# Kernel optimization log

Measured on AMD Instinct MI355X. Metric: run time of the kernel, lower is better.

Reference implementation:

```python
import jax, jax.numpy as jnp
import numpy as np

B = 256      # graph pairs
N = 256      # nodes per graph (uniform -> padding is a reshape)
DEG = 16     # avg degree
D = 32       # one_hot_dim
F1, F2, F3 = 128, 64, 64
T = 16       # tensor_neurons
BINS = 16
BOT = 16     # bottle_neck_neurons


def setup_inputs() -> dict:
    key = jax.random.key(0)
    ks = jax.random.split(key, 24)
    NT = B * N            # total nodes per side
    NE = B * N * DEG      # total directed edges per side
    x_q = jax.random.normal(ks[0], (NT, D), jnp.float32)
    x_c = jax.random.normal(ks[1], (NT, D), jnp.float32)
    edge_q = jax.random.randint(ks[2], (2, NE), 0, NT, jnp.int32)
    edge_c = jax.random.randint(ks[3], (2, NE), 0, NT, jnp.int32)
    qgraph_sizes = jnp.full((B,), N, jnp.int32)
    cgraph_sizes = jnp.full((B,), N, jnp.int32)

    def glorot(k, shape):
        fan = sum(shape[-2:]) if len(shape) >= 2 else shape[0] * 2
        return jax.random.uniform(k, shape, jnp.float32, -1.0, 1.0) * np.sqrt(6.0 / fan)

    params = dict(
        W1=glorot(ks[4], (D, F1)), b1=jnp.zeros((F1,), jnp.float32),
        W2=glorot(ks[5], (F1, F2)), b2=jnp.zeros((F2,), jnp.float32),
        W3=glorot(ks[6], (F2, F3)), b3=jnp.zeros((F3,), jnp.float32),
        attn_w=glorot(ks[7], (F3, F3)),
        ntn_a_w=glorot(ks[8], (T, F3, F3)),
        ntn_b_w=glorot(ks[9], (2 * F3, T)),
        ntn_bias=glorot(ks[10], (T, 1)),
        fc1_w=glorot(ks[11], (T + BINS, BOT)), fc1_b=jnp.zeros((BOT,), jnp.float32),
        fc2_w=glorot(ks[12], (BOT, 1)), fc2_b=jnp.zeros((1,), jnp.float32),
    )
    return dict(x_q=x_q, edge_q=edge_q, x_c=x_c, edge_c=edge_c,
                qgraph_sizes=qgraph_sizes, cgraph_sizes=cgraph_sizes, **params)


def _gcn(x, src, dst, W, b):
    n = x.shape[0]
    h = x @ W
    loop = jnp.arange(n, dtype=src.dtype)
    s = jnp.concatenate([src, loop])
    d = jnp.concatenate([dst, loop])
    deg = jax.ops.segment_sum(jnp.ones(s.shape, h.dtype), d, num_segments=n)
    dinv = jnp.where(deg > 0, jax.lax.rsqrt(jnp.maximum(deg, 1.0)), 0.0)
    coef = (dinv[s] * dinv[d])[:, None]
    return jax.ops.segment_sum(h[s] * coef, d, num_segments=n) + b


def _gnn(x, ei, W1, b1, W2, b2, W3, b3):
    src, dst = ei[0], ei[1]
    h = jax.nn.relu(_gcn(x, src, dst, W1, b1))        # dropout is identity in eval
    h = jax.nn.relu(_gcn(h, src, dst, W2, b2))
    return _gcn(h, src, dst, W3, b3)                  # [B*N, F3]


def _att_pool(q, attn_w, sizes):
    # q: [B, N, F3]
    ctx = jnp.tanh((q.sum(axis=1) @ attn_w) / sizes.astype(q.dtype)[:, None])  # [B, F3]
    sig = jax.nn.sigmoid(jnp.einsum('bnf,bf->bn', q, ctx))                      # [B, N]
    return jnp.einsum('bnf,bn->bf', q, sig)                                     # [B, F3]


def _pair_hist(q, c):
    # per-pair histogram of q @ c^T with BINS bins over each pair's [min, max]
    s = jax.lax.stop_gradient(jnp.einsum('bnf,bmf->bnm', q, c))  # [B, N, N]
    mn = s.min(axis=(1, 2), keepdims=True)
    mx = s.max(axis=(1, 2), keepdims=True)
    idx = jnp.clip(jnp.floor((s - mn) / jnp.maximum(mx - mn, 1e-12) * BINS),
                   0, BINS - 1).astype(jnp.int32)
    gid = (idx + jnp.arange(B, dtype=jnp.int32)[:, None, None] * BINS).reshape(-1)
    h = jax.ops.segment_sum(jnp.ones(gid.shape, jnp.float32), gid,
                            num_segments=B * BINS).reshape(B, BINS)
    return h / h.sum(axis=1, keepdims=True)


def reference(x_q, edge_q, x_c, edge_c, qgraph_sizes, cgraph_sizes,
              W1, b1, W2, b2, W3, b3, attn_w, ntn_a_w, ntn_b_w, ntn_bias,
              fc1_w, fc1_b, fc2_w, fc2_b):
    q = _gnn(x_q, edge_q, W1, b1, W2, b2, W3, b3).reshape(B, N, F3)
    c = _gnn(x_c, edge_c, W1, b1, W2, b2, W3, b3).reshape(B, N, F3)
    e1 = _att_pool(q, attn_w, qgraph_sizes)
    e2 = _att_pool(c, attn_w, cgraph_sizes)
    ntn = (jnp.einsum('bi,tij,bj->bt', e1, ntn_a_w, e2)
           + jnp.concatenate([e1, e2], axis=-1) @ ntn_b_w
           + ntn_bias[:, 0])
    scores = jax.nn.relu(ntn)                                   # [B, T]
    hist = _pair_hist(q, c)                                     # [B, BINS]
    scores = jnp.concatenate([scores, hist], axis=1)
    scores = jax.nn.relu(scores @ fc1_w + fc1_b)
    p = jax.nn.sigmoid(scores @ fc2_w + fc2_b)[:, 0]            # [B]
    ged = -0.5 * (qgraph_sizes + cgraph_sizes).astype(p.dtype) * jnp.log(p)
    return ged
```

## Files before the change

### kernel.cpp

```cpp
#include <hip/hip_runtime.h>
#include <hip/hip_bf16.h>
#include <math.h>

#define BB 256
#define NN 256
#define NT (BB*NN)
#define NT2 (2*NT)
#define NE (NT*16)
#define DD 32
#define F1C 128
#define F2C 64
#define F3C 64
#define TT 16
#define BINS 16

#define NBUCK 256
#define BSHIFT 9
#define BNODES 512
#define BCAP 10240
#define EPB 4096

typedef __attribute__((ext_vector_type(8))) short short8;
typedef __attribute__((ext_vector_type(4))) float f32x4;
typedef __attribute__((ext_vector_type(2))) float f32x2;

__device__ inline float b2f(ushort u) { return __uint_as_float(((uint)u) << 16); }
__device__ inline ushort f2b(float f) {
    uint u = __float_as_uint(f);
    return (ushort)((u + 0x7fffu + ((u >> 16) & 1u)) >> 16);
}
__device__ inline float clamp8(float v) { return fminf(fmaxf(v, -448.0f), 448.0f); }
__device__ inline uchar f2f8(float v) {
    int r = __builtin_amdgcn_cvt_pk_fp8_f32(clamp8(v), 0.0f, 0, false);
    return (uchar)(r & 0xff);
}
__device__ inline void f8x8_acc(uint2 w, float* acc) {
    f32x2 p;
    p = __builtin_amdgcn_cvt_pk_f32_fp8(w.x, false); acc[0] += p.x; acc[1] += p.y;
    p = __builtin_amdgcn_cvt_pk_f32_fp8(w.x, true);  acc[2] += p.x; acc[3] += p.y;
    p = __builtin_amdgcn_cvt_pk_f32_fp8(w.y, false); acc[4] += p.x; acc[5] += p.y;
    p = __builtin_amdgcn_cvt_pk_f32_fp8(w.y, true);  acc[6] += p.x; acc[7] += p.y;
}
__device__ inline uint2 f8x8_pack(const float* v) {
    uint2 r;
    r.x = (uint)__builtin_amdgcn_cvt_pk_fp8_f32(clamp8(v[0]), clamp8(v[1]), 0, false);
    r.x = (uint)__builtin_amdgcn_cvt_pk_fp8_f32(clamp8(v[2]), clamp8(v[3]), (int)r.x, true);
    r.y = (uint)__builtin_amdgcn_cvt_pk_fp8_f32(clamp8(v[4]), clamp8(v[5]), 0, false);
    r.y = (uint)__builtin_amdgcn_cvt_pk_fp8_f32(clamp8(v[6]), clamp8(v[7]), (int)r.y, true);
    return r;
}

__global__ __launch_bounds__(256) void zero_k(int* __restrict__ gcount) {
    gcount[threadIdx.x] = 0;
}

__global__ __launch_bounds__(256) void csr_p1_k(const int* __restrict__ eq, const int* __restrict__ ec,
                                                uint* __restrict__ staged, int* __restrict__ gcount) {
    __shared__ uint s_pk[EPB];
    __shared__ int s_cnt[NBUCK];
    __shared__ int s_off[NBUCK];
    __shared__ int s_base[NBUCK];
    __shared__ int s_gb[NBUCK];
    int t = threadIdx.x;
    bool sideB = blockIdx.x >= 256;
    const int* edge = sideB ? ec : eq;
    int off = sideB ? NT : 0;
    int e0 = (blockIdx.x & 255) * EPB;
    s_cnt[t] = 0;
    __syncthreads();
    uint pk[16]; int bk[16];
#pragma unroll
    for (int j = 0; j < 16; j++) {
        int e = e0 + j * 256 + t;
        int s = edge[e] + off;
        int d = edge[NE + e] + off;
        bk[j] = d >> BSHIFT;
        pk[j] = ((uint)s << BSHIFT) | (uint)(d & (BNODES - 1));
        atomicAdd(&s_cnt[bk[j]], 1);
    }
    __syncthreads();
    s_off[t] = s_cnt[t];
    __syncthreads();
    for (int o = 1; o < NBUCK; o <<= 1) {
        int x = (t >= o) ? s_off[t - o] : 0;
        __syncthreads();
        s_off[t] += x;
        __syncthreads();
    }
    {
        int ex = s_off[t] - s_cnt[t];
        s_base[t] = ex;
        s_off[t] = ex;
        s_gb[t] = atomicAdd(&gcount[t], s_cnt[t]);
    }
    __syncthreads();
#pragma unroll
    for (int j = 0; j < 16; j++) {
        int pos = atomicAdd(&s_off[bk[j]], 1);
        s_pk[pos] = pk[j];
    }
    __syncthreads();
    int w = t >> 6, l = t & 63;
    int bsel = l >> 4, l16 = l & 15;
    for (int pb = w; pb < NBUCK / 4; pb += 4) {
        int b = pb * 4 + bsel;
        int n = s_cnt[b], st = s_base[b], gb = s_gb[b];
        if (gb + n > BCAP) n = max(0, BCAP - gb);
        for (int i = l16; i < n; i += 16)
            staged[b * BCAP + gb + i] = s_pk[st + i];
    }
}

__global__ __launch_bounds__(256) void csr_p2_k(const uint* __restrict__ staged, const int* __restrict__ gcount,
                                                int* __restrict__ rp, int* __restrict__ indeg,
                                                float* __restrict__ dinv, int* __restrict__ ep) {
    int b = blockIdx.x;
    int t = threadIdx.x;
    __shared__ int cnt[BNODES];
    __shared__ int fl[BNODES];
    __shared__ int wsum[256];
    __shared__ int gsc[NBUCK];
    cnt[t] = 0; cnt[t + 256] = 0;
    gsc[t] = min(gcount[t], BCAP);
    __syncthreads();
    for (int off = 1; off < NBUCK; off <<= 1) {
        int x = (t >= off) ? gsc[t - off] : 0;
        __syncthreads();
        gsc[t] += x;
        __syncthreads();
    }
    int gbase = (b == 0) ? 0 : gsc[b - 1];
    int n = min(gcount[b], BCAP);
    const uint* sb = staged + (size_t)b * BCAP;
    int i = t;
    for (; i + 768 < n; i += 1024) {
        uint p0 = sb[i];
        uint p1 = sb[i + 256];
        uint p2 = sb[i + 512];
        uint p3 = sb[i + 768];
        atomicAdd(&cnt[p0 & (BNODES - 1)], 1);
        atomicAdd(&cnt[p1 & (BNODES - 1)], 1);
        atomicAdd(&cnt[p2 & (BNODES - 1)], 1);
        atomicAdd(&cnt[p3 & (BNODES - 1)], 1);
    }
    for (; i < n; i += 256)
        atomicAdd(&cnt[sb[i] & (BNODES - 1)], 1);
    __syncthreads();
    int base2 = t * 2;
    int c0 = cnt[base2], c1 = cnt[base2 + 1];
    int s2 = c0 + c1;
    wsum[t] = s2;
    __syncthreads();
    for (int off = 1; off < 256; off <<= 1) {
        int x = (t >= off) ? wsum[t - off] : 0;
        __syncthreads();
        wsum[t] += x;
        __syncthreads();
    }
    int p = gbase + wsum[t] - s2;
    int v0 = b * BNODES + base2;
    rp[v0] = p;          fl[base2] = p;
    indeg[v0] = c0;      dinv[v0] = rsqrtf((float)(c0 + 1));
    p += c0;
    rp[v0 + 1] = p;      fl[base2 + 1] = p;
    indeg[v0 + 1] = c1;  dinv[v0 + 1] = rsqrtf((float)(c1 + 1));
    __syncthreads();
    i = t;
    for (; i + 768 < n; i += 1024) {
        uint p0 = sb[i];
        uint p1 = sb[i + 256];
        uint p2 = sb[i + 512];
        uint p3 = sb[i + 768];
        ep[atomicAdd(&fl[p0 & (BNODES - 1)], 1)] = (int)(p0 >> BSHIFT);
        ep[atomicAdd(&fl[p1 & (BNODES - 1)], 1)] = (int)(p1 >> BSHIFT);
        ep[atomicAdd(&fl[p2 & (BNODES - 1)], 1)] = (int)(p2 >> BSHIFT);
        ep[atomicAdd(&fl[p3 & (BNODES - 1)], 1)] = (int)(p3 >> BSHIFT);
    }
    for (; i < n; i += 256) {
        uint pk = sb[i];
        ep[atomicAdd(&fl[pk & (BNODES - 1)], 1)] = (int)(pk >> BSHIFT);
    }
}

__global__ __launch_bounds__(256) void cvt2w_k(const float* __restrict__ a, const float* __restrict__ b,
                                               const float* __restrict__ dinv, ushort* __restrict__ out,
                                               const float* __restrict__ W1, const float* __restrict__ W2,
                                               const float* __restrict__ W3, ushort* __restrict__ Wt1,
                                               ushort* __restrict__ Wt2, uchar* __restrict__ Wt3f8) {
    const int NB_X = NT2 * DD / 4 / 256;
    if (blockIdx.x < NB_X) {
        int i = blockIdx.x * 256 + threadIdx.x;
        const int per = NT * DD / 4;
        bool sideB = i >= per;
        const float4* src = (const float4*)(sideB ? b : a);
        float4 v = src[sideB ? i - per : i];
        float dv = dinv[i / (DD / 4)];
        ushort4 o;
        o.x = f2b(v.x * dv); o.y = f2b(v.y * dv); o.z = f2b(v.z * dv); o.w = f2b(v.w * dv);
        ((ushort4*)out)[i] = o;
    } else {
        int i = (blockIdx.x - NB_X) * 256 + threadIdx.x;
        if (i < DD * F1C)  { int k = i / F1C, n = i % F1C; Wt1[n * DD + k]  = f2b(W1[i]); }
        if (i < F1C * F2C) { int k = i / F2C, n = i % F2C; Wt2[n * F1C + k] = f2b(W2[i]); }
        if (i < F2C * F3C) { int k = i / F3C, n = i % F3C; Wt3f8[n * F2C + k] = f2f8(W3[i]); }
    }
}

template<int F, bool BIAS, bool RELU>
__global__ __launch_bounds__(256) void agg_bf_k(const ushort* __restrict__ in, const int* __restrict__ rp,
                                                const int* __restrict__ indeg, const int* __restrict__ ep,
                                                const float* __restrict__ dinv,
                                                const float* __restrict__ bias, ushort* __restrict__ out) {
    constexpr int LPV = F / 8;
    constexpr int VPB = 256 / LPV;
    int g = threadIdx.x / LPV;
    int l = threadIdx.x % LPV;
    int v = blockIdx.x * VPB + g;
    float dv = dinv[v];
    short8 rs = *(const short8*)(in + (size_t)v * F + l * 8);
    float acc[8];
#pragma unroll
    for (int j = 0; j < 8; j++) acc[j] = b2f((ushort)rs[j]);
    int start = rp[v];
    int cnt   = indeg[v];
    int i = 0;
    for (; i + 4 <= cnt; i += 4) {
        int s0 = ep[start + i];
        int s1 = ep[start + i + 1];
        int s2 = ep[start + i + 2];
        int s3 = ep[start + i + 3];
        short8 r0 = *(const short8*)(in + (size_t)s0 * F + l * 8);
        short8 r1 = *(const short8*)(in + (size_t)s1 * F + l * 8);
        short8 r2 = *(const short8*)(in + (size_t)s2 * F + l * 8);
        short8 r3 = *(const short8*)(in + (size_t)s3 * F + l * 8);
#pragma unroll
        for (int j = 0; j < 8; j++) {
            acc[j] += b2f((ushort)r0[j]);
            acc[j] += b2f((ushort)r1[j]);
            acc[j] += b2f((ushort)r2[j]);
            acc[j] += b2f((ushort)r3[j]);
        }
    }
    for (; i < cnt; i++) {
        int s0 = ep[start + i];
        short8 r0 = *(const short8*)(in + (size_t)s0 * F + l * 8);
#pragma unroll
        for (int j = 0; j < 8; j++) acc[j] += b2f((ushort)r0[j]);
    }
    short8 o;
#pragma unroll
    for (int j = 0; j < 8; j++) {
        float x = dv * acc[j];
        if (BIAS) x += bias[l * 8 + j];
        if (RELU) x = fmaxf(x, 0.0f);
        o[j] = (short)f2b(x);
    }
    *(short8*)(out + (size_t)v * F + l * 8) = o;
}

template<bool OUT_BF16, bool BIAS, bool RELU>
__global__ __launch_bounds__(256) void agg_f8_k(const uchar* __restrict__ in, const int* __restrict__ rp,
                                                const int* __restrict__ indeg, const int* __restrict__ ep,
                                                const float* __restrict__ dinv,
                                                const float* __restrict__ bias, void* __restrict__ outp) {
    int g = threadIdx.x >> 3;
    int l = threadIdx.x & 7;
    int v = blockIdx.x * 32 + g;
    float dv = dinv[v];
    float acc[8] = {0, 0, 0, 0, 0, 0, 0, 0};
    f8x8_acc(*(const uint2*)(in + (size_t)v * 64 + l * 8), acc);
    int start = rp[v];
    int cnt   = indeg[v];
    int i = 0;
    for (; i + 4 <= cnt; i += 4) {
        int s0 = ep[start + i];
        int s1 = ep[start + i + 1];
        int s2 = ep[start + i + 2];
        int s3 = ep[start + i + 3];
        uint2 g0 = *(const uint2*)(in + (size_t)s0 * 64 + l * 8);
        uint2 g1 = *(const uint2*)(in + (size_t)s1 * 64 + l * 8);
        uint2 g2 = *(const uint2*)(in + (size_t)s2 * 64 + l * 8);
        uint2 g3 = *(const uint2*)(in + (size_t)s3 * 64 + l * 8);
        f8x8_acc(g0, acc); f8x8_acc(g1, acc); f8x8_acc(g2, acc); f8x8_acc(g3, acc);
    }
    for (; i < cnt; i++) {
        int s0 = ep[start + i];
        f8x8_acc(*(const uint2*)(in + (size_t)s0 * 64 + l * 8), acc);
    }
#pragma unroll
    for (int j = 0; j < 8; j++) {
        float x = dv * acc[j];
        if (BIAS) x += bias[l * 8 + j];
        if (RELU) x = fmaxf(x, 0.0f);
        acc[j] = x;
    }
    if (OUT_BF16) {
        short8 o;
#pragma unroll
        for (int j = 0; j < 8; j++) o[j] = (short)f2b(acc[j]);
        *(short8*)((ushort*)outp + (size_t)v * 64 + l * 8) = o;
    } else {
        *(uint2*)((uchar*)outp + (size_t)v * 64 + l * 8) = f8x8_pack(acc);
    }
}

__global__ __launch_bounds__(256) void gemm12_k(const ushort* __restrict__ xa,
                                                const ushort* __restrict__ Wt1,
                                                const float* __restrict__ b1,
                                                const ushort* __restrict__ Wt2,
                                                const float* __restrict__ dinv,
                                                uchar* __restrict__ h8a) {
    __shared__ ushort s_h1[128][136];
    int w = threadIdx.x >> 6, lane = threadIdx.x & 63;
    int r16 = lane & 15, quad = lane >> 4, koff = quad * 8;
    size_t rows0 = (size_t)blockIdx.x * 128;

    short8 af1[2];
#pragma unroll
    for (int mt = 0; mt < 2; mt++)
        af1[mt] = *(const short8*)(xa + (rows0 + (w * 2 + mt) * 16 + r16) * 32 + koff);
#pragma unroll
    for (int nt = 0; nt < 8; nt++) {
        short8 bfr = *(const short8*)(Wt1 + (size_t)(nt * 16 + r16) * 32 + koff);
        f32x4 acc[2] = {{0.f,0.f,0.f,0.f},{0.f,0.f,0.f,0.f}};
        acc[0] = __builtin_amdgcn_mfma_f32_16x16x32_bf16(af1[0], bfr, acc[0], 0, 0, 0);
        acc[1] = __builtin_amdgcn_mfma_f32_16x16x32_bf16(af1[1], bfr, acc[1], 0, 0, 0);
        int col = nt * 16 + r16;
        float bc = b1[col];
#pragma unroll
        for (int mt = 0; mt < 2; mt++)
#pragma unroll
            for (int r = 0; r < 4; r++) {
                int rl = (w * 2 + mt) * 16 + quad * 4 + r;
                s_h1[rl][col] = f2b(fmaxf(acc[mt][r] + bc, 0.0f));
            }
    }
    __syncthreads();

    short8 af2[4][2];
#pragma unroll
    for (int kc = 0; kc < 4; kc++)
#pragma unroll
        for (int mt = 0; mt < 2; mt++)
            af2[kc][mt] = *(const short8*)&s_h1[(w * 2 + mt) * 16 + r16][kc * 32 + koff];
    float dvr[2][4];
#pragma unroll
    for (int mt = 0; mt < 2; mt++)
#pragma unroll
        for (int r = 0; r < 4; r++)
            dvr[mt][r] = dinv[rows0 + (w * 2 + mt) * 16 + quad * 4 + r];
#pragma unroll
    for (int nt = 0; nt < 4; nt++) {
        f32x4 acc[2] = {{0.f,0.f,0.f,0.f},{0.f,0.f,0.f,0.f}};
#pragma unroll
        for (int kc = 0; kc < 4; kc++) {
            short8 bfr = *(const short8*)(Wt2 + (size_t)(nt * 16 + r16) * 128 + kc * 32 + koff);
            acc[0] = __builtin_amdgcn_mfma_f32_16x16x32_bf16(af2[kc][0], bfr, acc[0], 0, 0, 0);
            acc[1] = __builtin_amdgcn_mfma_f32_16x16x32_bf16(af2[kc][1], bfr, acc[1], 0, 0, 0);
        }
#pragma unroll
        for (int mt = 0; mt < 2; mt++)
#pragma unroll
            for (int r = 0; r < 4; r++) {
                size_t row = rows0 + (w * 2 + mt) * 16 + quad * 4 + r;
                int col = nt * 16 + r16;
                h8a[row * 64 + col] = f2f8(acc[mt][r] * dvr[mt][r]);
            }
    }
}

__global__ __launch_bounds__(256) void gemm_f8_k(const uchar* __restrict__ A8,
                                                 const uchar* __restrict__ Wt8,
                                                 const float* __restrict__ dinv,
                                                 uchar* __restrict__ out8) {
    int w = threadIdx.x >> 6, lane = threadIdx.x & 63;
    int r16 = lane & 15, koff = (lane >> 4) * 8;
    size_t rows0 = (size_t)blockIdx.x * 128;

    long af[2][2];
#pragma unroll
    for (int kc = 0; kc < 2; kc++)
#pragma unroll
        for (int mt = 0; mt < 2; mt++)
            af[kc][mt] = *(const long*)(A8 + (rows0 + (w * 2 + mt) * 16 + r16) * 64 + kc * 32 + koff);

    float dvr[2][4];
#pragma unroll
    for (int mt = 0; mt < 2; mt++)
#pragma unroll
        for (int r = 0; r < 4; r++)
            dvr[mt][r] = dinv[rows0 + (w * 2 + mt) * 16 + (lane >> 4) * 4 + r];

#pragma unroll
    for (int nt = 0; nt < 4; nt++) {
        f32x4 acc[2] = {{0.f,0.f,0.f,0.f},{0.f,0.f,0.f,0.f}};
#pragma unroll
        for (int kc = 0; kc < 2; kc++) {
            long b = *(const long*)(Wt8 + (size_t)(nt * 16 + r16) * 64 + kc * 32 + koff);
            acc[0] = __builtin_amdgcn_mfma_f32_16x16x32_fp8_fp8(af[kc][0], b, acc[0], 0, 0, 0);
            acc[1] = __builtin_amdgcn_mfma_f32_16x16x32_fp8_fp8(af[kc][1], b, acc[1], 0, 0, 0);
        }
#pragma unroll
        for (int mt = 0; mt < 2; mt++) {
#pragma unroll
            for (int r = 0; r < 4; r++) {
                size_t row = rows0 + (w * 2 + mt) * 16 + (lane >> 4) * 4 + r;
                int col = nt * 16 + (lane & 15);
                out8[row * 64 + col] = f2f8(acc[mt][r] * dvr[mt][r]);
            }
        }
    }
}

__global__ __launch_bounds__(256) void pool_hist_k(const ushort* __restrict__ fin,
                                                   const int* __restrict__ qsz, const int* __restrict__ csz,
                                                   const float* __restrict__ attn_w,
                                                   float* __restrict__ e_out, float* __restrict__ histp) {
    __shared__ float smemf[17472];
    int t = threadIdx.x;
    if (blockIdx.x < 512) {
        int b = blockIdx.x & 255;
        bool is_c = blockIdx.x >= BB;
        const ushort* emb = fin + (size_t)blockIdx.x * NN * F3C;
        float size = (float)((is_c ? csz : qsz)[b]);
        float* eo = e_out + (is_c ? BB * F3C : 0) + b * F3C;
        float (*s_emb)[F3C + 1] = (float(*)[F3C + 1])smemf;
        float* s_red = smemf + 256 * 65;
        float* s_sq  = s_red + 256;
        float* s_ctx = s_sq + 64;
        float* s_sig = s_ctx + 64;
        int f = t & 63;
        int w = t >> 6;
        float psum = 0.0f;
        for (int n = w; n < NN; n += 4) {
            float v = b2f(emb[n * F3C + f]);
            s_emb[n][f] = v;
            psum += v;
        }
        s_red[w * 64 + f] = psum;
        __syncthreads();
        if (w == 0) {
            s_sq[f] = s_red[f] + s_red[64 + f] + s_red[128 + f] + s_red[192 + f];
            float acc = 0.0f;
            for (int k = 0; k < 64; k++) acc += s_sq[k] * attn_w[k * 64 + f];
            s_ctx[f] = tanhf(acc / size);
        }
        __syncthreads();
        {
            float acc = 0.0f;
#pragma unroll 8
            for (int k = 0; k < 64; k++) acc += s_emb[t][k] * s_ctx[k];
            s_sig[t] = 1.0f / (1.0f + expf(-acc));
        }
        __syncthreads();
        float eacc = 0.0f;
#pragma unroll 8
        for (int i = 0; i < 64; i++) {
            int n = w * 64 + i;
            eacc += s_sig[n] * s_emb[n][f];
        }
        s_red[w * 64 + f] = eacc;
        __syncthreads();
        if (w == 0) eo[f] = s_red[f] + s_red[64 + f] + s_red[128 + f] + s_red[192 + f];
    } else {
        int b = blockIdx.x - 512;
        const ushort* qb = fin + (size_t)b * NN * 64;
        const ushort* cb = fin + (size_t)(NT + b * NN) * 64;
        int lane = t & 63;
        int w = t >> 6;
        int r16 = lane & 15, koff = (lane >> 4) * 8;
        int* h = (int*)smemf;
        int* hp = h + 16 * 256;
        float* smn = (float*)(hp + 256);
        float* smx = smn + 4;
        float* s_sc = smx + 4;

        short8 a[4][2];
#pragma unroll
        for (int i = 0; i < 4; i++) {
            int row = (w * 4 + i) * 16 + r16;
#pragma unroll
            for (int kk = 0; kk < 2; kk++)
                a[i][kk] = *(const short8*)(qb + row * 64 + kk * 32 + koff);
        }
        float mn = 1e30f, mx = -1e30f;
        for (int mt = 0; mt < 16; mt++) {
            int crow = mt * 16 + r16;
            short8 b0 = *(const short8*)(cb + crow * 64 + koff);
            short8 b1 = *(const short8*)(cb + crow * 64 + 32 + koff);
#pragma unroll
            for (int i = 0; i < 4; i++) {
                f32x4 acc = {0.0f, 0.0f, 0.0f, 0.0f};
                acc = __builtin_amdgcn_mfma_f32_16x16x32_bf16(a[i][0], b0, acc, 0, 0, 0);
                acc = __builtin_amdgcn_mfma_f32_16x16x32_bf16(a[i][1], b1, acc, 0, 0, 0);
                mn = fminf(mn, fminf(fminf(acc[0], acc[1]), fminf(acc[2], acc[3])));
                mx = fmaxf(mx, fmaxf(fmaxf(acc[0], acc[1]), fmaxf(acc[2], acc[3])));
            }
        }
        for (int off = 32; off; off >>= 1) {
            mn = fminf(mn, __shfl_xor(mn, off, 64));
            mx = fmaxf(mx, __shfl_xor(mx, off, 64));
        }
        if (lane == 0) { smn[w] = mn; smx[w] = mx; }
        __syncthreads();
        if (t == 0) {
            float m0 = fminf(fminf(smn[0], smn[1]), fminf(smn[2], smn[3]));
            float m1 = fmaxf(fmaxf(smx[0], smx[1]), fmaxf(smx[2], smx[3]));
            s_sc[0] = m0;
            s_sc[1] = 16.0f / fmaxf(m1 - m0, 1e-12f);
        }
#pragma unroll
        for (int i = 0; i < 16; i++) h[i * 256 + t] = 0;
        __syncthreads();
        float bmn = s_sc[0], bscale = s_sc[1];
        for (int mt = 0; mt < 16; mt++) {
            int crow = mt * 16 + r16;
            short8 b0 = *(const short8*)(cb + crow * 64 + koff);
            short8 b1 = *(const short8*)(cb + crow * 64 + 32 + koff);
#pragma unroll
            for (int i = 0; i < 4; i++) {
                f32x4 acc = {0.0f, 0.0f, 0.0f, 0.0f};
                acc = __builtin_amdgcn_mfma_f32_16x16x32_bf16(a[i][0], b0, acc, 0, 0, 0);
                acc = __builtin_amdgcn_mfma_f32_16x16x32_bf16(a[i][1], b1, acc, 0, 0, 0);
#pragma unroll
                for (int r = 0; r < 4; r++) {
                    int bin = (int)floorf((acc[r] - bmn) * bscale);
                    bin = min(max(bin, 0), 15);
                    h[bin * 256 + t] += 1;
                }
            }
        }
        __syncthreads();
        int bb = t >> 4, part = t & 15;
        int sum = 0;
#pragma unroll
        for (int j = 0; j < 16; j++) sum += h[bb * 256 + part * 16 + j];
        hp[bb * 16 + part] = sum;
        __syncthreads();
        if (t < 16) {
            int s = 0;
#pragma unroll
            for (int j = 0; j < 16; j++) s += hp[t * 16 + j];
            histp[b * 16 + t] = (float)s;
        }
    }
}

__global__ __launch_bounds__(256) void ntn_final_k(const float* __restrict__ e, const float* __restrict__ A,
                                                   const float* __restrict__ bw, const float* __restrict__ bias,
                                                   const float* __restrict__ histp,
                                                   const float* __restrict__ fc1w, const float* __restrict__ fc1b,
                                                   const float* __restrict__ fc2w, const float* __restrict__ fc2b,
                                                   const int* __restrict__ qsz, const int* __restrict__ csz,
                                                   float* __restrict__ out) {
    int b = blockIdx.x;
    int t = threadIdx.x;
    __shared__ float s_e1[64], s_e2[64];
    __shared__ float s_ntn[16];
    __shared__ float s_s[32];
    __shared__ float s_a[16];
    if (t < 64) s_e1[t] = e[b * 64 + t];
    else if (t < 128) s_e2[t - 64] = e[BB * 64 + b * 64 + (t - 64)];
    if (t < 16) s_ntn[t] = 0.0f;
    __syncthreads();
#pragma unroll
    for (int r = 0; r < 4; r++) {
        int idx = t + r * 256;
        int tt = idx >> 6, i = idx & 63;
        const float* Ar = A + (size_t)idx * 64;
        float acc = 0.0f;
        for (int j = 0; j < 64; j++) acc += Ar[j] * s_e2[j];
        atomicAdd(&s_ntn[tt], s_e1[i] * acc);
    }
    __syncthreads();
    if (t < 16) {
        float acc = s_ntn[t] + bias[t];
        for (int k = 0; k < 64; k++) acc += s_e1[k] * bw[k * 16 + t];
        for (int k = 0; k < 64; k++) acc += s_e2[k] * bw[(64 + k) * 16 + t];
        s_s[t] = fmaxf(acc, 0.0f);
        s_s[16 + t] = histp[b * 16 + t] * (1.0f / 65536.0f);
    }
    __syncthreads();
    if (t < 16) {
        float a = fc1b[t];
        for (int k = 0; k < 32; k++) a += s_s[k] * fc1w[k * 16 + t];
        s_a[t] = fmaxf(a, 0.0f);
    }
    __syncthreads();
    if (t == 0) {
        float z = fc2b[0];
        for (int j = 0; j < 16; j++) z += s_a[j] * fc2w[j];
        float nz = -z;
        float sp = (nz > 20.0f) ? nz : log1pf(expf(nz));
        out[b] = 0.5f * (float)(qsz[b] + csz[b]) * sp;
    }
}

extern "C" void kernel_launch(void* const* d_in, const int* in_sizes, int n_in,
                              void* d_out, int out_size, void* d_ws, size_t ws_size,
                              hipStream_t stream) {
    const float* x_q    = (const float*)d_in[0];
    const int*   edge_q = (const int*)d_in[1];
    const float* x_c    = (const float*)d_in[2];
    const int*   edge_c = (const int*)d_in[3];
    const int*   qsz    = (const int*)d_in[4];
    const int*   csz    = (const int*)d_in[5];
    const float* W1 = (const float*)d_in[6];
    const float* b1 = (const float*)d_in[7];
    const float* W2 = (const float*)d_in[8];
    const float* b2 = (const float*)d_in[9];
    const float* W3 = (const float*)d_in[10];
    const float* b3 = (const float*)d_in[11];
    const float* attn_w  = (const float*)d_in[12];
    const float* ntn_a   = (const float*)d_in[13];
    const float* ntn_b   = (const float*)d_in[14];
    const float* ntn_bias= (const float*)d_in[15];
    const float* fc1w = (const float*)d_in[16];
    const float* fc1b = (const float*)d_in[17];
    const float* fc2w = (const float*)d_in[18];
    const float* fc2b = (const float*)d_in[19];
    float* out = (float*)d_out;

    char* w = (char*)d_ws;
    auto alloc = [&](size_t bytes) -> void* {
        void* p = (void*)w;
        w += (bytes + 255) & ~(size_t)255;
        return p;
    };
    int*    rp     = (int*)alloc((size_t)NT2 * 4);
    int*    indeg  = (int*)alloc((size_t)NT2 * 4);
    float*  dinv   = (float*)alloc((size_t)NT2 * 4);
    int*    gcount = (int*)alloc(NBUCK * 4);
    uint*   staged = (uint*)alloc((size_t)NBUCK * BCAP * 4);
    int*    ep     = (int*)alloc((size_t)2 * NE * 4);
    ushort* xb     = (ushort*)alloc((size_t)NT2 * 32 * 2);
    ushort* xa     = (ushort*)alloc((size_t)NT2 * 32 * 2);
    uchar*  h8a    = (uchar*)alloc((size_t)NT2 * 64);
    uchar*  h8b    = (uchar*)alloc((size_t)NT2 * 64);
    ushort* fin    = (ushort*)alloc((size_t)NT2 * 64 * 2);
    ushort* Wt1    = (ushort*)alloc((size_t)DD * F1C * 2);
    ushort* Wt2    = (ushort*)alloc((size_t)F1C * F2C * 2);
    uchar*  Wt3f8  = (uchar*)alloc((size_t)F2C * F3C);
    float*  e12    = (float*)alloc(2 * BB * 64 * 4);
    float*  histp  = (float*)alloc(256 * 16 * 4);

    zero_k<<<1, 256, 0, stream>>>(gcount);
    csr_p1_k<<<512, 256, 0, stream>>>(edge_q, edge_c, staged, gcount);
    csr_p2_k<<<NBUCK, 256, 0, stream>>>(staged, gcount, rp, indeg, dinv, ep);

    cvt2w_k<<<NT2 * 32 / 4 / 256 + 64, 256, 0, stream>>>(x_q, x_c, dinv, xb,
                                                         W1, W2, W3, Wt1, Wt2, Wt3f8);

    agg_bf_k<32, false, false><<<NT2 / 64, 256, 0, stream>>>(xb, rp, indeg, ep, dinv, nullptr, xa);
    gemm12_k<<<NT2 / 128, 256, 0, stream>>>(xa, Wt1, b1, Wt2, dinv, h8a);
    agg_f8_k<false, true, true><<<NT2 / 32, 256, 0, stream>>>(h8a, rp, indeg, ep, dinv, b2, h8b);
    gemm_f8_k<<<NT2 / 128, 256, 0, stream>>>(h8b, Wt3f8, dinv, h8a);
    agg_f8_k<true, true, false><<<NT2 / 32, 256, 0, stream>>>(h8a, rp, indeg, ep, dinv, b3, fin);

    pool_hist_k<<<768, 256, 0, stream>>>(fin, qsz, csz, attn_w, e12, histp);
    ntn_final_k<<<BB, 256, 0, stream>>>(e12, ntn_a, ntn_b, ntn_bias, histp,
                                        fc1w, fc1b, fc2w, fc2b, qsz, csz, out);
}
```

Before: 306.5 us.

## Split fused pool/histogram kernel into pool, min-max and binning kernels

The single pool_hist kernel is split into three kernels. pool_k does the attention pooling. hist_mm_k computes partial min and max over quarter tiles of the pair similarity matrix. hist_bin_k recomputes the products and bins them, adding its counts into an integer histogram with atomics. The pair histogram work now runs on four times as many blocks, which should improve load balance and occupancy, since the old 256 histogram blocks were heavier than the pool blocks. The cost is two extra launches, recomputing the MFMA products, and atomics, with the histogram buffer zeroed in zero_k.

```diff
diff --git a/kernel.cpp b/kernel.cpp
--- a/kernel.cpp
+++ b/kernel.cpp
@@ -50,8 +50,10 @@
     return r;
 }
 
-__global__ __launch_bounds__(256) void zero_k(int* __restrict__ gcount) {
-    gcount[threadIdx.x] = 0;
+__global__ __launch_bounds__(256) void zero_k(int* __restrict__ gcount, int* __restrict__ histp) {
+    int i = blockIdx.x * 256 + threadIdx.x;
+    if (i < NBUCK) gcount[i] = 0;
+    if (i < BB * BINS) histp[i] = 0;
 }
 
 __global__ __launch_bounds__(256) void csr_p1_k(const int* __restrict__ eq, const int* __restrict__ ec,
@@ -412,143 +414,152 @@
     }
 }
 
-__global__ __launch_bounds__(256) void pool_hist_k(const ushort* __restrict__ fin,
-                                                   const int* __restrict__ qsz, const int* __restrict__ csz,
-                                                   const float* __restrict__ attn_w,
-                                                   float* __restrict__ e_out, float* __restrict__ histp) {
-    __shared__ float smemf[17472];
+__global__ __launch_bounds__(256) void pool_k(const ushort* __restrict__ fin,
+                                              const int* __restrict__ qsz, const int* __restrict__ csz,
+                                              const float* __restrict__ attn_w, float* __restrict__ e_out) {
+    int b = blockIdx.x & 255;
+    bool is_c = blockIdx.x >= BB;
+    const ushort* emb = fin + (size_t)blockIdx.x * NN * F3C;
+    float size = (float)((is_c ? csz : qsz)[b]);
+    float* eo = e_out + (is_c ? BB * F3C : 0) + b * F3C;
+
     int t = threadIdx.x;
-    if (blockIdx.x < 512) {
-        int b = blockIdx.x & 255;
-        bool is_c = blockIdx.x >= BB;
-        const ushort* emb = fin + (size_t)blockIdx.x * NN * F3C;
-        float size = (float)((is_c ? csz : qsz)[b]);
-        float* eo = e_out + (is_c ? BB * F3C : 0) + b * F3C;
-        float (*s_emb)[F3C + 1] = (float(*)[F3C + 1])smemf;
-        float* s_red = smemf + 256 * 65;
-        float* s_sq  = s_red + 256;
-        float* s_ctx = s_sq + 64;
-        float* s_sig = s_ctx + 64;
-        int f = t & 63;
-        int w = t >> 6;
-        float psum = 0.0f;
-        for (int n = w; n < NN; n += 4) {
-            float v = b2f(emb[n * F3C + f]);
-            s_emb[n][f] = v;
-            psum += v;
+    int f = t & 63;
+    int w = t >> 6;
+
+    __shared__ float s_emb[NN][F3C + 1];
+    __shared__ float s_red[4][64];
+    __shared__ float s_sq[64];
+    __shared__ float s_ctx[64];
+    __shared__ float s_sig[NN];
+
+    float psum = 0.0f;
+    for (int n = w; n < NN; n += 4) {
+        float v = b2f(emb[n * F3C + f]);
+        s_emb[n][f] = v;
+        psum += v;
+    }
+    s_red[w][f] = psum;
+    __syncthreads();
+
+    if (w == 0) {
+        s_sq[f] = s_red[0][f] + s_red[1][f] + s_red[2][f] + s_red[3][f];
+        float acc = 0.0f;
+        for (int k = 0; k < 64; k++) acc += s_sq[k] * attn_w[k * 64 + f];
+        s_ctx[f] = tanhf(acc / size);
+    }
+    __syncthreads();
+
+    {
+        float acc = 0.0f;
+#pragma unroll 8
+        for (int k = 0; k < 64; k++) acc += s_emb[t][k] * s_ctx[k];
+        s_sig[t] = 1.0f / (1.0f + expf(-acc));
+    }
+    __syncthreads();
+
+    float eacc = 0.0f;
+#pragma unroll 8
+    for (int i = 0; i < 64; i++) {
+        int n = w * 64 + i;
+        eacc += s_sig[n] * s_emb[n][f];
+    }
+    s_red[w][f] = eacc;
+    __syncthreads();
+    if (w == 0) eo[f] = s_red[0][f] + s_red[1][f] + s_red[2][f] + s_red[3][f];
+}
+
+__global__ __launch_bounds__(256) void hist_mm_k(const ushort* __restrict__ fin,
+                                                 float* __restrict__ pmn, float* __restrict__ pmx) {
+    int b = blockIdx.x >> 2, quarter = blockIdx.x & 3;
+    const ushort* qb = fin + (size_t)b * NN * 64;
+    const ushort* cb = fin + (size_t)(NT + b * NN) * 64;
+    int lane = threadIdx.x & 63;
+    int w = threadIdx.x >> 6;
+    int r16 = lane & 15, koff = (lane >> 4) * 8;
+    int qrow = quarter * 64 + w * 16 + r16;
+    short8 a0 = *(const short8*)(qb + qrow * 64 + koff);
+    short8 a1 = *(const short8*)(qb + qrow * 64 + 32 + koff);
+
+    float mn = 1e30f, mx = -1e30f;
+    for (int mt = 0; mt < 16; mt++) {
+        int crow = mt * 16 + r16;
+        short8 b0 = *(const short8*)(cb + crow * 64 + koff);
+        short8 b1 = *(const short8*)(cb + crow * 64 + 32 + koff);
+        f32x4 acc = {0.0f, 0.0f, 0.0f, 0.0f};
+        acc = __builtin_amdgcn_mfma_f32_16x16x32_bf16(a0, b0, acc, 0, 0, 0);
+        acc = __builtin_amdgcn_mfma_f32_16x16x32_bf16(a1, b1, acc, 0, 0, 0);
+        mn = fminf(mn, fminf(fminf(acc[0], acc[1]), fminf(acc[2], acc[3])));
+        mx = fmaxf(mx, fmaxf(fmaxf(acc[0], acc[1]), fmaxf(acc[2], acc[3])));
+    }
+    for (int off = 32; off; off >>= 1) {
+        mn = fminf(mn, __shfl_xor(mn, off, 64));
+        mx = fmaxf(mx, __shfl_xor(mx, off, 64));
+    }
+    __shared__ float smn[4], smx[4];
+    if (lane == 0) { smn[w] = mn; smx[w] = mx; }
+    __syncthreads();
+    if (threadIdx.x == 0) {
+        pmn[blockIdx.x] = fminf(fminf(smn[0], smn[1]), fminf(smn[2], smn[3]));
+        pmx[blockIdx.x] = fmaxf(fmaxf(smx[0], smx[1]), fmaxf(smx[2], smx[3]));
+    }
+}
+
+__global__ __launch_bounds__(256) void hist_bin_k(const ushort* __restrict__ fin,
+                                                  const float* __restrict__ pmn, const float* __restrict__ pmx,
+                                                  int* __restrict__ histp) {
+    int b = blockIdx.x >> 2, quarter = blockIdx.x & 3;
+    const ushort* qb = fin + (size_t)b * NN * 64;
+    const ushort* cb = fin + (size_t)(NT + b * NN) * 64;
+    int lane = threadIdx.x & 63;
+    int w = threadIdx.x >> 6;
+    int r16 = lane & 15, koff = (lane >> 4) * 8;
+    int qrow = quarter * 64 + w * 16 + r16;
+    short8 a0 = *(const short8*)(qb + qrow * 64 + koff);
+    short8 a1 = *(const short8*)(qb + qrow * 64 + 32 + koff);
+
+    float mn = fminf(fminf(pmn[4 * b], pmn[4 * b + 1]), fminf(pmn[4 * b + 2], pmn[4 * b + 3]));
+    float mx = fmaxf(fmaxf(pmx[4 * b], pmx[4 * b + 1]), fmaxf(pmx[4 * b + 2], pmx[4 * b + 3]));
+    float scale = 16.0f / fmaxf(mx - mn, 1e-12f);
+
+    __shared__ int h[16 * 256];
+#pragma unroll
+    for (int i = 0; i < 16; i++) h[i * 256 + threadIdx.x] = 0;
+    __syncthreads();
+
+    for (int mt = 0; mt < 16; mt++) {
+        int crow = mt * 16 + r16;
+        short8 b0 = *(const short8*)(cb + crow * 64 + koff);
+        short8 b1 = *(const short8*)(cb + crow * 64 + 32 + koff);
+        f32x4 acc = {0.0f, 0.0f, 0.0f, 0.0f};
+        acc = __builtin_amdgcn_mfma_f32_16x16x32_bf16(a0, b0, acc, 0, 0, 0);
+        acc = __builtin_amdgcn_mfma_f32_16x16x32_bf16(a1, b1, acc, 0, 0, 0);
+#pragma unroll
+        for (int r = 0; r < 4; r++) {
+            int bin = (int)floorf((acc[r] - mn) * scale);
+            bin = min(max(bin, 0), 15);
+            h[bin * 256 + threadIdx.x] += 1;
         }
-        s_red[w * 64 + f] = psum;
-        __syncthreads();
-        if (w == 0) {
-            s_sq[f] = s_red[f] + s_red[64 + f] + s_red[128 + f] + s_red[192 + f];
-            float acc = 0.0f;
-            for (int k = 0; k < 64; k++) acc += s_sq[k] * attn_w[k * 64 + f];
-            s_ctx[f] = tanhf(acc / size);
-        }
-        __syncthreads();
-        {
-            float acc = 0.0f;
-#pragma unroll 8
-            for (int k = 0; k < 64; k++) acc += s_emb[t][k] * s_ctx[k];
-            s_sig[t] = 1.0f / (1.0f + expf(-acc));
-        }
-        __syncthreads();
-        float eacc = 0.0f;
-#pragma unroll 8
-        for (int i = 0; i < 64; i++) {
-            int n = w * 64 + i;
-            eacc += s_sig[n] * s_emb[n][f];
-        }
-        s_red[w * 64 + f] = eacc;
-        __syncthreads();
-        if (w == 0) eo[f] = s_red[f] + s_red[64 + f] + s_red[128 + f] + s_red[192 + f];
-    } else {
-        int b = blockIdx.x - 512;
-        const ushort* qb = fin + (size_t)b * NN * 64;
-        const ushort* cb = fin + (size_t)(NT + b * NN) * 64;
-        int lane = t & 63;
-        int w = t >> 6;
-        int r16 = lane & 15, koff = (lane >> 4) * 8;
-        int* h = (int*)smemf;
-        int* hp = h + 16 * 256;
-        float* smn = (float*)(hp + 256);
-        float* smx = smn + 4;
-        float* s_sc = smx + 4;
-
-        short8 a[4][2];
-#pragma unroll
-        for (int i = 0; i < 4; i++) {
-            int row = (w * 4 + i) * 16 + r16;
-#pragma unroll
-            for (int kk = 0; kk < 2; kk++)
-                a[i][kk] = *(const short8*)(qb + row * 64 + kk * 32 + koff);
-        }
-        float mn = 1e30f, mx = -1e30f;
-        for (int mt = 0; mt < 16; mt++) {
-            int crow = mt * 16 + r16;
-            short8 b0 = *(const short8*)(cb + crow * 64 + koff);
-            short8 b1 = *(const short8*)(cb + crow * 64 + 32 + koff);
-#pragma unroll
-            for (int i = 0; i < 4; i++) {
-                f32x4 acc = {0.0f, 0.0f, 0.0f, 0.0f};
-                acc = __builtin_amdgcn_mfma_f32_16x16x32_bf16(a[i][0], b0, acc, 0, 0, 0);
-                acc = __builtin_amdgcn_mfma_f32_16x16x32_bf16(a[i][1], b1, acc, 0, 0, 0);
-                mn = fminf(mn, fminf(fminf(acc[0], acc[1]), fminf(acc[2], acc[3])));
-                mx = fmaxf(mx, fmaxf(fmaxf(acc[0], acc[1]), fmaxf(acc[2], acc[3])));
-            }
-        }
-        for (int off = 32; off; off >>= 1) {
-            mn = fminf(mn, __shfl_xor(mn, off, 64));
-            mx = fmaxf(mx, __shfl_xor(mx, off, 64));
-        }
-        if (lane == 0) { smn[w] = mn; smx[w] = mx; }
-        __syncthreads();
-        if (t == 0) {
-            float m0 = fminf(fminf(smn[0], smn[1]), fminf(smn[2], smn[3]));
-            float m1 = fmaxf(fmaxf(smx[0], smx[1]), fmaxf(smx[2], smx[3]));
-            s_sc[0] = m0;
-            s_sc[1] = 16.0f / fmaxf(m1 - m0, 1e-12f);
-        }
-#pragma unroll
-        for (int i = 0; i < 16; i++) h[i * 256 + t] = 0;
-        __syncthreads();
-        float bmn = s_sc[0], bscale = s_sc[1];
-        for (int mt = 0; mt < 16; mt++) {
-            int crow = mt * 16 + r16;
-            short8 b0 = *(const short8*)(cb + crow * 64 + koff);
-            short8 b1 = *(const short8*)(cb + crow * 64 + 32 + koff);
-#pragma unroll
-            for (int i = 0; i < 4; i++) {
-                f32x4 acc = {0.0f, 0.0f, 0.0f, 0.0f};
-                acc = __builtin_amdgcn_mfma_f32_16x16x32_bf16(a[i][0], b0, acc, 0, 0, 0);
-                acc = __builtin_amdgcn_mfma_f32_16x16x32_bf16(a[i][1], b1, acc, 0, 0, 0);
-#pragma unroll
-                for (int r = 0; r < 4; r++) {
-                    int bin = (int)floorf((acc[r] - bmn) * bscale);
-                    bin = min(max(bin, 0), 15);
-                    h[bin * 256 + t] += 1;
-                }
-            }
-        }
-        __syncthreads();
-        int bb = t >> 4, part = t & 15;
-        int sum = 0;
-#pragma unroll
-        for (int j = 0; j < 16; j++) sum += h[bb * 256 + part * 16 + j];
-        hp[bb * 16 + part] = sum;
-        __syncthreads();
-        if (t < 16) {
-            int s = 0;
-#pragma unroll
-            for (int j = 0; j < 16; j++) s += hp[t * 16 + j];
-            histp[b * 16 + t] = (float)s;
-        }
+    }
+    __syncthreads();
+    __shared__ int hp[16][16];
+    int bb = threadIdx.x >> 4, part = threadIdx.x & 15;
+    int sum = 0;
+#pragma unroll
+    for (int j = 0; j < 16; j++) sum += h[bb * 256 + part * 16 + j];
+    hp[bb][part] = sum;
+    __syncthreads();
+    if (threadIdx.x < 16) {
+        int s = 0;
+#pragma unroll
+        for (int j = 0; j < 16; j++) s += hp[threadIdx.x][j];
+        atomicAdd(&histp[b * 16 + threadIdx.x], s);
     }
 }
 
 __global__ __launch_bounds__(256) void ntn_final_k(const float* __restrict__ e, const float* __restrict__ A,
                                                    const float* __restrict__ bw, const float* __restrict__ bias,
-                                                   const float* __restrict__ histp,
+                                                   const int* __restrict__ histp,
                                                    const float* __restrict__ fc1w, const float* __restrict__ fc1b,
                                                    const float* __restrict__ fc2w, const float* __restrict__ fc2b,
                                                    const int* __restrict__ qsz, const int* __restrict__ csz,
@@ -578,7 +589,7 @@
         for (int k = 0; k < 64; k++) acc += s_e1[k] * bw[k * 16 + t];
         for (int k = 0; k < 64; k++) acc += s_e2[k] * bw[(64 + k) * 16 + t];
         s_s[t] = fmaxf(acc, 0.0f);
-        s_s[16 + t] = histp[b * 16 + t] * (1.0f / 65536.0f);
+        s_s[16 + t] = (float)histp[b * 16 + t] * (1.0f / 65536.0f);
     }
     __syncthreads();
     if (t < 16) {
@@ -642,9 +653,11 @@
     ushort* Wt2    = (ushort*)alloc((size_t)F1C * F2C * 2);
     uchar*  Wt3f8  = (uchar*)alloc((size_t)F2C * F3C);
     float*  e12    = (float*)alloc(2 * BB * 64 * 4);
-    float*  histp  = (float*)alloc(256 * 16 * 4);
-
-    zero_k<<<1, 256, 0, stream>>>(gcount);
+    float*  pmn    = (float*)alloc(1024 * 4);
+    float*  pmx    = (float*)alloc(1024 * 4);
+    int*    histp  = (int*)alloc(BB * BINS * 4);
+
+    zero_k<<<16, 256, 0, stream>>>(gcount, histp);
     csr_p1_k<<<512, 256, 0, stream>>>(edge_q, edge_c, staged, gcount);
     csr_p2_k<<<NBUCK, 256, 0, stream>>>(staged, gcount, rp, indeg, dinv, ep);
 
@@ -657,7 +670,9 @@
     gemm_f8_k<<<NT2 / 128, 256, 0, stream>>>(h8b, Wt3f8, dinv, h8a);
     agg_f8_k<true, true, false><<<NT2 / 32, 256, 0, stream>>>(h8a, rp, indeg, ep, dinv, b3, fin);
 
-    pool_hist_k<<<768, 256, 0, stream>>>(fin, qsz, csz, attn_w, e12, histp);
+    pool_k<<<512, 256, 0, stream>>>(fin, qsz, csz, attn_w, e12);
+    hist_mm_k<<<1024, 256, 0, stream>>>(fin, pmn, pmx);
+    hist_bin_k<<<1024, 256, 0, stream>>>(fin, pmn, pmx, histp);
     ntn_final_k<<<BB, 256, 0, stream>>>(e12, ntn_a, ntn_b, ntn_bias, histp,
                                         fc1w, fc1b, fc2w, fc2b, qsz, csz, out);
 }
```

Result: slower. 318.5 us (+3.9%).

## Batch edge gathers by eight and stage embeddings in LDS with vectorized loads

Applied to the files above, without the earlier changes.

The fp8 aggregation kernel gains an 8-wide gather loop so more independent neighbour loads are in flight per thread. The attention-pool branch now loads bf16 embeddings with 16-byte vector loads into shared memory and sums from LDS, replacing strided scalar global reads. The histogram branch copies the c-graph tile into padded shared memory once and reads MFMA B operands from LDS in both passes instead of re-reading global memory. The cost is extra register pressure for the 8-wide gather and added LDS traffic and barriers.

```diff
diff --git a/kernel.cpp b/kernel.cpp
--- a/kernel.cpp
+++ b/kernel.cpp
@@ -272,6 +272,16 @@
     int start = rp[v];
     int cnt   = indeg[v];
     int i = 0;
+    for (; i + 8 <= cnt; i += 8) {
+        int sx[8];
+#pragma unroll
+        for (int j = 0; j < 8; j++) sx[j] = ep[start + i + j];
+        uint2 gx[8];
+#pragma unroll
+        for (int j = 0; j < 8; j++) gx[j] = *(const uint2*)(in + (size_t)sx[j] * 64 + l * 8);
+#pragma unroll
+        for (int j = 0; j < 8; j++) f8x8_acc(gx[j], acc);
+    }
     for (; i + 4 <= cnt; i += 4) {
         int s0 = ep[start + i];
         int s1 = ep[start + i + 1];
@@ -431,12 +441,18 @@
         float* s_sig = s_ctx + 64;
         int f = t & 63;
         int w = t >> 6;
+#pragma unroll
+        for (int it = 0; it < 8; it++) {
+            int idx = it * 2048 + t * 8;
+            int row = idx >> 6, f0 = idx & 63;
+            short8 v = *(const short8*)(emb + idx);
+#pragma unroll
+            for (int j = 0; j < 8; j++) s_emb[row][f0 + j] = b2f((ushort)v[j]);
+        }
+        __syncthreads();
         float psum = 0.0f;
-        for (int n = w; n < NN; n += 4) {
-            float v = b2f(emb[n * F3C + f]);
-            s_emb[n][f] = v;
-            psum += v;
-        }
+#pragma unroll 8
+        for (int i2 = 0; i2 < 64; i2++) psum += s_emb[w * 64 + i2][f];
         s_red[w * 64 + f] = psum;
         __syncthreads();
         if (w == 0) {
@@ -469,12 +485,19 @@
         int lane = t & 63;
         int w = t >> 6;
         int r16 = lane & 15, koff = (lane >> 4) * 8;
-        int* h = (int*)smemf;
+        ushort (*cb_s)[72] = (ushort(*)[72])smemf;
+        int* h = (int*)(smemf + 9216);
         int* hp = h + 16 * 256;
         float* smn = (float*)(hp + 256);
         float* smx = smn + 4;
         float* s_sc = smx + 4;
 
+#pragma unroll
+        for (int it = 0; it < 8; it++) {
+            int idx = it * 2048 + t * 8;
+            int row = idx >> 6, f0 = idx & 63;
+            *(short8*)&cb_s[row][f0] = *(const short8*)(cb + idx);
+        }
         short8 a[4][2];
 #pragma unroll
         for (int i = 0; i < 4; i++) {
@@ -483,11 +506,12 @@
             for (int kk = 0; kk < 2; kk++)
                 a[i][kk] = *(const short8*)(qb + row * 64 + kk * 32 + koff);
         }
+        __syncthreads();
         float mn = 1e30f, mx = -1e30f;
         for (int mt = 0; mt < 16; mt++) {
             int crow = mt * 16 + r16;
-            short8 b0 = *(const short8*)(cb + crow * 64 + koff);
-            short8 b1 = *(const short8*)(cb + crow * 64 + 32 + koff);
+            short8 b0 = *(const short8*)&cb_s[crow][koff];
+            short8 b1 = *(const short8*)&cb_s[crow][32 + koff];
 #pragma unroll
             for (int i = 0; i < 4; i++) {
                 f32x4 acc = {0.0f, 0.0f, 0.0f, 0.0f};
@@ -515,8 +539,8 @@
         float bmn = s_sc[0], bscale = s_sc[1];
         for (int mt = 0; mt < 16; mt++) {
             int crow = mt * 16 + r16;
-            short8 b0 = *(const short8*)(cb + crow * 64 + koff);
-            short8 b1 = *(const short8*)(cb + crow * 64 + 32 + koff);
+            short8 b0 = *(const short8*)&cb_s[crow][koff];
+            short8 b1 = *(const short8*)&cb_s[crow][32 + koff];
 #pragma unroll
             for (int i = 0; i < 4; i++) {
                 f32x4 acc = {0.0f, 0.0f, 0.0f, 0.0f};
```

Measured after the change: 285.6 us. 6.8% less time.
